# Optimization experiments

Measured on AMD Instinct MI355X. Metric: run time of the kernel, lower is better.

## Reference

```python
import jax, jax.numpy as jnp
import numpy as np

B = 32
H = W = 64
C = 128
HEADS = 4
HEAD_DIM = C // HEADS
WS = 8            # window_size
SS = 4            # shift_size
N = WS * WS       # tokens per window
MLP_HID = 4 * C
SCALE = HEAD_DIM ** -0.5
EPS = 1e-5


def _rel_pos_index():
    coords = np.stack(np.meshgrid(np.arange(WS), np.arange(WS), indexing='ij'))
    cf = coords.reshape(2, -1)
    rel = (cf[:, :, None] - cf[:, None, :]).transpose(1, 2, 0)
    rel[:, :, 0] += WS - 1
    rel[:, :, 1] += WS - 1
    rel[:, :, 0] *= 2 * WS - 1
    return rel.sum(-1)  # (N, N) int


def _attn_mask():
    img_mask = np.zeros((1, H, W, 1), np.float32)
    slices = (slice(0, -WS), slice(-WS, -SS), slice(-SS, None))
    cnt = 0
    for hs in slices:
        for ws in slices:
            img_mask[:, hs, ws, :] = cnt
            cnt += 1
    mw = img_mask.reshape(1, H // WS, WS, W // WS, WS, 1)
    mw = mw.transpose(0, 1, 3, 2, 4, 5).reshape(-1, N)  # (nW, N)
    am = mw[:, None, :] - mw[:, :, None]
    return np.where(am != 0, np.float32(-100.0), np.float32(0.0))  # (nW, N, N)


REL_POS_IDX = jnp.asarray(_rel_pos_index().reshape(-1))  # (N*N,)
ATTN_MASK = jnp.asarray(_attn_mask())                    # (nW, N, N)


def setup_inputs() -> dict:
    key = jax.random.key(0)
    ks = jax.random.split(key, 12)
    s = 0.02
    return {
        'x': jax.random.normal(ks[0], (B, H * W, C), jnp.float32),
        'norm1_g': jnp.ones((C,), jnp.float32),
        'norm1_b': jnp.zeros((C,), jnp.float32),
        'qkv_w': jax.random.normal(ks[1], (C, 3 * C), jnp.float32) * s,
        'qkv_b': jnp.zeros((3 * C,), jnp.float32),
        'proj_w': jax.random.normal(ks[2], (C, C), jnp.float32) * s,
        'proj_b': jnp.zeros((C,), jnp.float32),
        'rpb_table': jax.random.normal(ks[3], ((2 * WS - 1) * (2 * WS - 1), HEADS), jnp.float32) * s,
        'norm2_g': jnp.ones((C,), jnp.float32),
        'norm2_b': jnp.zeros((C,), jnp.float32),
        'mlp_w1': jax.random.normal(ks[4], (C, MLP_HID), jnp.float32) * s,
        'mlp_b1': jnp.zeros((MLP_HID,), jnp.float32),
        'mlp_w2': jax.random.normal(ks[5], (MLP_HID, C), jnp.float32) * s,
        'mlp_b2': jnp.zeros((C,), jnp.float32),
    }


def _layernorm(x, g, b):
    m = x.mean(-1, keepdims=True)
    v = jnp.mean((x - m) ** 2, -1, keepdims=True)
    return (x - m) * jax.lax.rsqrt(v + EPS) * g + b


def reference(x, norm1_g, norm1_b, qkv_w, qkv_b, proj_w, proj_b, rpb_table,
              norm2_g, norm2_b, mlp_w1, mlp_b1, mlp_w2, mlp_b2):
    shortcut = x
    h = _layernorm(x, norm1_g, norm1_b).reshape(-1, H, W, C)
    # cyclic shift
    h = jnp.roll(h, (-SS, -SS), axis=(1, 2))
    # window partition -> (B*nW, N, C)
    hw = h.reshape(-1, H // WS, WS, W // WS, WS, C)
    hw = hw.transpose(0, 1, 3, 2, 4, 5).reshape(-1, N, C)
    # window attention
    qkv = (hw @ qkv_w + qkv_b).reshape(-1, N, 3, HEADS, HEAD_DIM)
    qkv = qkv.transpose(2, 0, 3, 1, 4)  # (3, B*nW, heads, N, hd)
    q, k, v = qkv[0] * SCALE, qkv[1], qkv[2]
    attn = jnp.einsum('bhnd,bhmd->bhnm', q, k)  # (B*nW, heads, N, N)
    rpb = rpb_table[REL_POS_IDX].reshape(N, N, HEADS).transpose(2, 0, 1)
    attn = attn + rpb[None]
    nW = ATTN_MASK.shape[0]
    attn = attn.reshape(-1, nW, HEADS, N, N) + ATTN_MASK[None, :, None]
    attn = jax.nn.softmax(attn.reshape(-1, HEADS, N, N), axis=-1)
    out = jnp.einsum('bhnm,bhmd->bhnd', attn, v)
    out = out.transpose(0, 2, 1, 3).reshape(-1, N, C)
    out = out @ proj_w + proj_b
    # window reverse
    out = out.reshape(-1, H // WS, W // WS, WS, WS, C)
    out = out.transpose(0, 1, 3, 2, 4, 5).reshape(-1, H, W, C)
    # reverse cyclic shift
    out = jnp.roll(out, (SS, SS), axis=(1, 2)).reshape(-1, H * W, C)
    x = shortcut + out
    # MLP branch
    h2 = _layernorm(x, norm2_g, norm2_b)
    h2 = jax.nn.gelu(h2 @ mlp_w1 + mlp_b1, approximate=False)
    h2 = h2 @ mlp_w2 + mlp_b2
    return x + h2
```

## Files before the change

kernel.cpp:

```cpp
#include <hip/hip_runtime.h>
#include <math.h>

typedef __attribute__((ext_vector_type(8))) short bf16x8;
typedef __attribute__((ext_vector_type(4))) short bf16x4;
typedef __attribute__((ext_vector_type(4))) float f32x4;
typedef __attribute__((ext_vector_type(4))) unsigned short u16x4;

#define DEVI __device__ __forceinline__

DEVI float b2f(unsigned int u){ union{unsigned int i; float f;} c; c.i = u<<16; return c.f; }
DEVI unsigned short f2b(float f){
  union{float f; unsigned int i;} c; c.f = f;
  unsigned int r = c.i + 0x7fffu + ((c.i>>16)&1u);
  return (unsigned short)(r>>16);
}
DEVI unsigned int pack2(float a, float b){
  return (unsigned int)f2b(a) | ((unsigned int)f2b(b)<<16);
}
DEVI void unpack8(uint4 u, float* f){
  f[0]=b2f(u.x&0xffffu); f[1]=b2f(u.x>>16);
  f[2]=b2f(u.y&0xffffu); f[3]=b2f(u.y>>16);
  f[4]=b2f(u.z&0xffffu); f[5]=b2f(u.z>>16);
  f[6]=b2f(u.w&0xffffu); f[7]=b2f(u.w>>16);
}
DEVI f32x4 mfma16(bf16x8 a, bf16x8 b, f32x4 c){
  return __builtin_amdgcn_mfma_f32_16x16x32_bf16(a, b, c, 0, 0, 0);
}
DEVI f32x4 mfma16x16(bf16x4 a, bf16x4 b, f32x4 c){
#if __has_builtin(__builtin_amdgcn_mfma_f32_16x16x16bf16_1k)
  return __builtin_amdgcn_mfma_f32_16x16x16bf16_1k(a, b, c, 0, 0, 0);
#else
  f32x4 d = c;
  asm volatile("v_mfma_f32_16x16x16_bf16 %0, %1, %2, %0" : "+v"(d) : "v"(a), "v"(b));
  return d;
#endif
}
DEVI float gelu_fast(float u){
  const float y = 0.7978845608028654f*(u + 0.044715f*u*u*u);
  const float t = __expf(2.f*y);
  const float th = 1.f - 2.f/(t + 1.f);
  return 0.5f*u*(1.f + th);
}
DEVI int swzA(int row, int byi){ return row*256 + (byi ^ ((row&7)<<4)); }
DEVI int swzQ(int row, int byi){ return row*64  + (byi ^ (((row>>1)&3)<<4)); }
DEVI int swzO(int row, int byc){ return row*512 + (byc ^ ((row&7)<<4) ^ (((byc>>7)&3)<<5)); }

__global__ void k_prep(const float* __restrict__ qkvw, const float* __restrict__ projw,
                       const float* __restrict__ w1,   const float* __restrict__ w2,
                       const float* __restrict__ rpbt,
                       ushort* __restrict__ qkvF, ushort* __restrict__ projF,
                       ushort* __restrict__ w1F,  ushort* __restrict__ w2F,
                       ushort* __restrict__ rpbE)
{
  const int t = blockIdx.x*256 + threadIdx.x;
  const int l = t&63, fr = t>>6;
  const int l15 = l&15, l4 = l>>4;
  {
    const int head = t>>12, q = (t>>6)&63, k = t&63;
    const int di = (q>>3)-(k>>3)+7, dj = (q&7)-(k&7)+7;
    rpbE[t] = f2b(rpbt[(di*15+dj)*4 + head]);
  }
  {
    const int c = fr>>5, og = (fr>>2)&7, h = fr&3;
    const int oc = og*16 + l15, hid0 = c*64 + h*16 + l4*4;
    ushort* d = w2F + (size_t)fr*256 + l*4;
    #pragma unroll
    for(int e=0;e<4;e++) d[e] = f2b(w2[(size_t)(hid0+e)*128 + oc]);
  }
  if (fr < 128){
    const int c = fr>>4, hg = (fr>>2)&3, kk = fr&3;
    const int hid = c*64 + hg*16 + l15, k0 = kk*32 + l4*8;
    ushort* d = w1F + (size_t)fr*512 + l*8;
    #pragma unroll
    for(int e=0;e<8;e++) d[e] = f2b(w1[(size_t)(k0+e)*512 + hid]);
  }
  if (fr < 96){
    const int s3 = fr>>5, g = (fr>>2)&7, kk = fr&3;
    const int col = s3*128 + g*16 + l15, k0 = kk*32 + l4*8;
    ushort* d = qkvF + (size_t)fr*512 + l*8;
    #pragma unroll
    for(int e=0;e<8;e++) d[e] = f2b(qkvw[(size_t)(k0+e)*384 + col]);
  }
  if (fr < 32){
    const int g = fr>>2, kk = fr&3;
    const int col = g*16 + l15, k0 = kk*32 + l4*8;
    ushort* d = projF + (size_t)fr*512 + l*8;
    #pragma unroll
    for(int e=0;e<8;e++) d[e] = f2b(projw[(size_t)(k0+e)*128 + col]);
  }
}

__global__ __launch_bounds__(256,3) void k_attn(
    const float*  __restrict__ x,
    const float*  __restrict__ g1, const float* __restrict__ be1,
    const ushort* __restrict__ qkvF, const float* __restrict__ qkvb,
    const ushort* __restrict__ projF, const float* __restrict__ projb,
    const ushort* __restrict__ rpbE,
    ushort* __restrict__ x2w)
{
  __shared__ __align__(16) char smem[49152];
  const int tid  = threadIdx.x;
  const int wave = tid>>6, lane = tid&63;
  const int l15 = lane&15, l4 = lane>>4;
  const int wid = blockIdx.x;
  const int b   = wid>>6, wim = wid&63;
  const int wh  = wim>>3, wv = wim&7;

  char* const smA  = smem;
  char* const smQ  = smem + 16384 + wave*8192;
  char* const smK  = smQ + 4096;
  char* const smR  = smem + 16384;

  const f32x4 Z = {0.f,0.f,0.f,0.f};
  const int t_row = tid>>2;
  const int cg    = (tid&3)*32;
  const int ti_r = t_row>>3, tj_r = t_row&7;
  const int ho_r = (wh*8+ti_r+4)&63, wo_r = (wv*8+tj_r+4)&63;
  const size_t growbase = ((size_t)(b*4096 + ho_r*64 + wo_r))*128;

  {
    const float* src = x + growbase + cg;
    float v[32];
    #pragma unroll
    for(int q=0;q<8;q++){
      const float4 f4 = *(const float4*)(src + q*4);
      v[q*4+0]=f4.x; v[q*4+1]=f4.y; v[q*4+2]=f4.z; v[q*4+3]=f4.w;
    }
    float s=0.f, ss=0.f;
    #pragma unroll
    for(int e=0;e<32;e++){ s+=v[e]; ss+=v[e]*v[e]; }
    s += __shfl_xor(s,1); ss += __shfl_xor(ss,1);
    s += __shfl_xor(s,2); ss += __shfl_xor(ss,2);
    const float mean = s*(1.f/128.f);
    const float varv = fmaxf(ss*(1.f/128.f) - mean*mean, 0.f);
    const float rstd = rsqrtf(varv + 1e-5f);
    #pragma unroll
    for(int q=0;q<4;q++){
      const float4 ga = *(const float4*)(g1 +cg+q*8);
      const float4 gb = *(const float4*)(g1 +cg+q*8+4);
      const float4 ba = *(const float4*)(be1+cg+q*8);
      const float4 bb = *(const float4*)(be1+cg+q*8+4);
      const float* vp = v + q*8;
      uint4 pk;
      pk.x = pack2((vp[0]-mean)*rstd*ga.x+ba.x, (vp[1]-mean)*rstd*ga.y+ba.y);
      pk.y = pack2((vp[2]-mean)*rstd*ga.z+ba.z, (vp[3]-mean)*rstd*ga.w+ba.w);
      pk.z = pack2((vp[4]-mean)*rstd*gb.x+bb.x, (vp[5]-mean)*rstd*gb.y+bb.y);
      pk.w = pack2((vp[6]-mean)*rstd*gb.z+bb.z, (vp[7]-mean)*rstd*gb.w+bb.w);
      *(uint4*)(smA + swzA(t_row, cg*2 + q*16)) = pk;
    }
  }
  __syncthreads();

  const int headc = wave*32;
  bf16x4 Vf[4][2];

  {
    #pragma unroll
    for(int s3=0;s3<3;s3++){
      f32x4 acc[4][2];
      #pragma unroll
      for(int rt=0;rt<4;rt++){ acc[rt][0]=Z; acc[rt][1]=Z; }
      bf16x8 bfr[2][4];
      #pragma unroll
      for(int ct=0;ct<2;ct++)
        #pragma unroll
        for(int kk=0;kk<4;kk++)
          bfr[ct][kk] = *(const bf16x8*)(qkvF + (size_t)((s3*8 + wave*2 + ct)*4 + kk)*512 + lane*8);
      #pragma unroll
      for(int kk=0;kk<4;kk++){
        bf16x8 afr[4];
        #pragma unroll
        for(int rt=0;rt<4;rt++)
          afr[rt] = *(const bf16x8*)(smA + swzA(rt*16+l15, kk*64 + l4*16));
        #pragma unroll
        for(int rt=0;rt<4;rt++)
          #pragma unroll
          for(int ct=0;ct<2;ct++)
            acc[rt][ct] = mfma16(afr[rt], bfr[ct][kk], acc[rt][ct]);
      }
      #pragma unroll
      for(int ct=0;ct<2;ct++){
        const int hd = ct*16 + l15;
        const float bias = qkvb[s3*128 + headc + hd];
        if (s3==2){
          #pragma unroll
          for(int rt=0;rt<4;rt++){
            union { uint2 u; bf16x4 v; } cv;
            cv.u.x = pack2(acc[rt][ct][0]+bias, acc[rt][ct][1]+bias);
            cv.u.y = pack2(acc[rt][ct][2]+bias, acc[rt][ct][3]+bias);
            Vf[rt][ct] = cv.v;
          }
        } else {
          char* const dst = (s3==0) ? smQ : smK;
          const float sc = (s3==0) ? 0.17677669529663687f : 1.f;
          #pragma unroll
          for(int rt=0;rt<4;rt++){
            const int t0 = rt*16 + l4*4;
            #pragma unroll
            for(int j=0;j<4;j++)
              *(ushort*)(dst + swzQ(t0+j, hd*2)) = f2b((acc[rt][ct][j]+bias)*sc);
          }
        }
      }
    }
  }
  __syncthreads();

  f32x4 O[4][2];
  #pragma unroll
  for(int rt=0;rt<4;rt++){ O[rt][0]=Z; O[rt][1]=Z; }
  {
    bf16x8 kfr[4];
    #pragma unroll
    for(int g=0; g<4; ++g)
      kfr[g] = *(const bf16x8*)(smK + swzQ(g*16+l15, l4*16));
    const bool edge = (wh==7) || (wv==7);
    #pragma unroll
    for(int rt=0; rt<4; ++rt){
      const bf16x8 qf = *(const bf16x8*)(smQ + swzQ(rt*16+l15, l4*16));
      f32x4 S[4];
      #pragma unroll
      for(int g=0; g<4; ++g)
        S[g] = mfma16(kfr[g], qf, Z);
      const int q = rt*16 + l15;
      int regq = 0;
      if (edge){
        const int qi=q>>3, qj=q&7;
        regq = ((wh<7)?0:((qi<4)?1:2))*3 + ((wv<7)?0:((qj<4)?1:2));
      }
      const ushort* rbase = rpbE + wave*4096 + q*64 + l4*4;
      #pragma unroll
      for(int g=0; g<4; ++g){
        const u16x4 rb = *(const u16x4*)(rbase + g*16);
        #pragma unroll
        for(int j=0;j<4;j++){
          float add = b2f(rb[j]);
          if (edge){
            const int k = g*16 + l4*4 + j;
            const int ki=k>>3, kj=k&7;
            const int regk = ((wh<7)?0:((ki<4)?1:2))*3 + ((wv<7)?0:((kj<4)?1:2));
            if (regk != regq) add -= 100.f;
          }
          S[g][j] += add;
        }
      }
      float mx = -1e30f;
      #pragma unroll
      for(int g=0;g<4;g++)
        #pragma unroll
        for(int j=0;j<4;j++) mx = fmaxf(mx, S[g][j]);
      mx = fmaxf(mx, __shfl_xor(mx,16));
      mx = fmaxf(mx, __shfl_xor(mx,32));
      float sm = 0.f;
      #pragma unroll
      for(int g=0;g<4;g++)
        #pragma unroll
        for(int j=0;j<4;j++){ const float e = __expf(S[g][j]-mx); S[g][j]=e; sm+=e; }
      sm += __shfl_xor(sm,16);
      sm += __shfl_xor(sm,32);
      const float inv = 1.f/sm;
      #pragma unroll
      for(int g=0;g<4;g++){
        union { uint2 u; bf16x4 v; } cv;
        cv.u.x = pack2(S[g][0]*inv, S[g][1]*inv);
        cv.u.y = pack2(S[g][2]*inv, S[g][3]*inv);
        #pragma unroll
        for(int cvi=0;cvi<2;cvi++)
          O[rt][cvi] = mfma16x16(cv.v, Vf[g][cvi], O[rt][cvi]);
      }
    }
    #pragma unroll
    for(int rt=0;rt<4;rt++)
      #pragma unroll
      for(int cvi=0;cvi<2;cvi++)
        #pragma unroll
        for(int j=0;j<4;j++)
          *(ushort*)(smA + swzA(rt*16+l4*4+j, (headc + cvi*16 + l15)*2)) = f2b(O[rt][cvi][j]);
  }
  __syncthreads();

  {
    f32x4 PR[4][2];
    #pragma unroll
    for(int rt=0;rt<4;rt++){ PR[rt][0]=Z; PR[rt][1]=Z; }
    bf16x8 pb[2][4];
    #pragma unroll
    for(int ct=0;ct<2;ct++)
      #pragma unroll
      for(int kk=0;kk<4;kk++)
        pb[ct][kk] = *(const bf16x8*)(projF + (size_t)((wave*2+ct)*4 + kk)*512 + lane*8);
    #pragma unroll
    for(int kk=0;kk<4;kk++){
      bf16x8 afr[4];
      #pragma unroll
      for(int rt=0;rt<4;rt++)
        afr[rt] = *(const bf16x8*)(smA + swzA(rt*16+l15, kk*64 + l4*16));
      #pragma unroll
      for(int rt=0;rt<4;rt++)
        #pragma unroll
        for(int ct=0;ct<2;ct++)
          PR[rt][ct] = mfma16(afr[rt], pb[ct][kk], PR[rt][ct]);
    }
    #pragma unroll
    for(int ct=0;ct<2;ct++){
      const int col = headc + ct*16 + l15;
      const float bias = projb[col];
      #pragma unroll
      for(int rt=0;rt<4;rt++)
        #pragma unroll
        for(int j=0;j<4;j++)
          *(float*)(smR + swzO(rt*16+l4*4+j, col*4)) = PR[rt][ct][j] + bias;
    }
  }
  __syncthreads();

  {
    const float* xsrc = x + growbase + cg;
    ushort* drow = x2w + ((size_t)(wid*64 + t_row))*128 + cg;
    #pragma unroll
    for(int q=0;q<4;q++){
      const f32x4 oa = *(const f32x4*)(smR + swzO(t_row, (cg+q*8  )*4));
      const f32x4 ob = *(const f32x4*)(smR + swzO(t_row, (cg+q*8+4)*4));
      const float4 xa = *(const float4*)(xsrc + q*8);
      const float4 xb = *(const float4*)(xsrc + q*8+4);
      uint4 pk;
      pk.x = pack2(oa[0]+xa.x, oa[1]+xa.y);
      pk.y = pack2(oa[2]+xa.z, oa[3]+xa.w);
      pk.z = pack2(ob[0]+xb.x, ob[1]+xb.y);
      pk.w = pack2(ob[2]+xb.z, ob[3]+xb.w);
      *(uint4*)(drow + q*8) = pk;
    }
  }
}

__global__ __launch_bounds__(512,1) void k_mlp2(
    const ushort* __restrict__ x2w,
    const float* __restrict__ g2, const float* __restrict__ be2,
    const ushort* __restrict__ w1F, const float* __restrict__ bb1,
    const ushort* __restrict__ w2F, const float* __restrict__ bb2,
    float* __restrict__ outp)
{
  extern __shared__ __align__(16) char smem[];
  char* const smX  = smem;
  char* const smW0 = smem + 65536;
  char* const smW1 = smem + 98304;
  const int tid  = threadIdx.x;
  const int wave = tid>>6, lane = tid&63;
  const int l15 = lane&15, l4 = lane>>4;
  const int gblk = blockIdx.x;
  const f32x4 Z = {0.f,0.f,0.f,0.f};

  const ushort* const wsrc = (tid & 256) ? w2F : w1F;
  const int soff = (tid & 255) * 32;
  const int loff = ((tid & 256) ? 16384 : 0) + (tid & 255)*64;
  uint4 stg0, stg1, stg2, stg3;
  {
    const uint4* p = (const uint4*)(wsrc + soff);
    stg0 = p[0]; stg1 = p[1]; stg2 = p[2]; stg3 = p[3];
  }

  {
    const int sub = tid>>2;
    const int cg  = (tid&3)*32;
    #pragma unroll
    for(int p=0;p<2;++p){
      const int tk = p*128 + sub;
      const ushort* src = x2w + ((size_t)(gblk*256 + tk))*128 + cg;
      float v[32];
      unpack8(*(const uint4*)(src   ), v   );
      unpack8(*(const uint4*)(src+ 8), v+ 8);
      unpack8(*(const uint4*)(src+16), v+16);
      unpack8(*(const uint4*)(src+24), v+24);
      float s=0.f, ss=0.f;
      #pragma unroll
      for(int e=0;e<32;e++){ s+=v[e]; ss+=v[e]*v[e]; }
      s += __shfl_xor(s,1); ss += __shfl_xor(ss,1);
      s += __shfl_xor(s,2); ss += __shfl_xor(ss,2);
      const float mean = s*(1.f/128.f);
      const float varv = fmaxf(ss*(1.f/128.f) - mean*mean, 0.f);
      const float rstd = rsqrtf(varv + 1e-5f);
      #pragma unroll
      for(int q=0;q<4;q++){
        const float4 ga = *(const float4*)(g2 +cg+q*8);
        const float4 gb = *(const float4*)(g2 +cg+q*8+4);
        const float4 ba = *(const float4*)(be2+cg+q*8);
        const float4 bb = *(const float4*)(be2+cg+q*8+4);
        const float* vp = v + q*8;
        uint4 pk;
        pk.x = pack2((vp[0]-mean)*rstd*ga.x+ba.x, (vp[1]-mean)*rstd*ga.y+ba.y);
        pk.y = pack2((vp[2]-mean)*rstd*ga.z+ba.z, (vp[3]-mean)*rstd*ga.w+ba.w);
        pk.z = pack2((vp[4]-mean)*rstd*gb.x+bb.x, (vp[5]-mean)*rstd*gb.y+bb.y);
        pk.w = pack2((vp[6]-mean)*rstd*gb.z+bb.z, (vp[7]-mean)*rstd*gb.w+bb.w);
        *(uint4*)(smX + swzA(tk, cg*2 + q*16)) = pk;
      }
    }
  }
  {
    uint4* d = (uint4*)(smW0 + loff);
    d[0]=stg0; d[1]=stg1; d[2]=stg2; d[3]=stg3;
  }
  __syncthreads();

  f32x4 OA[8][2];
  #pragma unroll
  for(int ocg=0;ocg<8;++ocg){ OA[ocg][0]=Z; OA[ocg][1]=Z; }

  for (int c=0; c<8; ++c){
    char* const buf = (c&1) ? smW1 : smW0;
    if (c<7){
      const uint4* p = (const uint4*)(wsrc + (size_t)(c+1)*8192 + soff);
      stg0 = p[0]; stg1 = p[1]; stg2 = p[2]; stg3 = p[3];
    }
    const int hidb = c*64;
    #pragma unroll
    for (int tokg=0; tokg<2; ++tokg){
      const int trow = wave*32 + tokg*16 + l15;
      bf16x8 xf[4];
      #pragma unroll
      for(int kk=0;kk<4;++kk)
        xf[kk] = *(const bf16x8*)(smX + swzA(trow, kk*64 + l4*16));
      f32x4 acc1[4] = {Z,Z,Z,Z};
      #pragma unroll
      for(int hg=0; hg<4; ++hg)
        #pragma unroll
        for(int kk=0; kk<4; ++kk){
          const bf16x8 wf = *(const bf16x8*)(buf + (hg*4+kk)*1024 + lane*16);
          acc1[hg] = mfma16(wf, xf[kk], acc1[hg]);
        }
      bf16x4 Hf[4];
      #pragma unroll
      for(int hg=0; hg<4; ++hg){
        const float4 b4 = *(const float4*)(bb1 + hidb + hg*16 + l4*4);
        bf16x4 hv;
        hv[0] = (short)f2b(gelu_fast(acc1[hg][0]+b4.x));
        hv[1] = (short)f2b(gelu_fast(acc1[hg][1]+b4.y));
        hv[2] = (short)f2b(gelu_fast(acc1[hg][2]+b4.z));
        hv[3] = (short)f2b(gelu_fast(acc1[hg][3]+b4.w));
        Hf[hg] = hv;
      }
      #pragma unroll
      for(int ocg=0; ocg<8; ++ocg)
        #pragma unroll
        for(int hg=0; hg<4; ++hg){
          const bf16x4 w2f = *(const bf16x4*)(buf + 16384 + (ocg*4+hg)*512 + lane*8);
          OA[ocg][tokg] = mfma16x16(w2f, Hf[hg], OA[ocg][tokg]);
        }
    }
    if (c<7){
      char* const nbuf = (c&1) ? smW0 : smW1;
      uint4* d = (uint4*)(nbuf + loff);
      d[0]=stg0; d[1]=stg1; d[2]=stg2; d[3]=stg3;
    }
    __syncthreads();
  }

  {
    const int sub = tid>>2;
    const int cg  = (tid&3)*32;
    #pragma unroll
    for(int p=0;p<2;++p){
      const int tk = p*128 + sub;
      const uint4* src = (const uint4*)(x2w + ((size_t)(gblk*256 + tk))*128 + cg);
      #pragma unroll
      for(int q=0;q<4;q++) *(uint4*)(smX + swzA(tk, cg*2 + q*16)) = src[q];
    }
  }
  __syncthreads();
  #pragma unroll
  for(int tokg=0; tokg<2; ++tokg){
    const int tk  = wave*32 + tokg*16 + l15;
    const int wid = gblk*4 + (tk>>6);
    const int n   = tk & 63;
    const int bb  = wid>>6, wim = wid&63;
    const int wh  = wim>>3, wv = wim&7;
    const int ti  = n>>3,  tj = n&7;
    const int ho  = (wh*8+ti+4)&63, wo = (wv*8+tj+4)&63;
    float* const drow = outp + ((size_t)(bb*4096 + ho*64 + wo))*128;
    #pragma unroll
    for(int ocg=0; ocg<8; ++ocg){
      const int oc = ocg*16 + l4*4;
      const float4 b4 = *(const float4*)(bb2 + oc);
      const u16x4 xr = *(const u16x4*)(smX + swzA(tk, oc*2));
      f32x4 r = OA[ocg][tokg];
      r[0] += b4.x + b2f(xr[0]);
      r[1] += b4.y + b2f(xr[1]);
      r[2] += b4.z + b2f(xr[2]);
      r[3] += b4.w + b2f(xr[3]);
      __builtin_nontemporal_store(r, (f32x4*)(drow + oc));
    }
  }
}

extern "C" void kernel_launch(void* const* d_in, const int* in_sizes, int n_in,
                              void* d_out, int out_size, void* d_ws, size_t ws_size,
                              hipStream_t stream) {
  (void)in_sizes; (void)n_in; (void)out_size; (void)ws_size;
  const float* x     = (const float*)d_in[0];
  const float* n1g   = (const float*)d_in[1];
  const float* n1b   = (const float*)d_in[2];
  const float* qkvw  = (const float*)d_in[3];
  const float* qkvb  = (const float*)d_in[4];
  const float* projw = (const float*)d_in[5];
  const float* projb = (const float*)d_in[6];
  const float* rpbt  = (const float*)d_in[7];
  const float* n2g   = (const float*)d_in[8];
  const float* n2b   = (const float*)d_in[9];
  const float* w1    = (const float*)d_in[10];
  const float* b1    = (const float*)d_in[11];
  const float* w2    = (const float*)d_in[12];
  const float* b2    = (const float*)d_in[13];
  float* outp = (float*)d_out;

  ushort* ws    = (ushort*)d_ws;
  ushort* x2w   = ws;
  ushort* qkvF  = ws + 16777216;
  ushort* projF = qkvF + 49152;
  ushort* w1F   = projF + 16384;
  ushort* w2F   = w1F + 65536;
  ushort* rpbE  = w2F + 65536;

  k_prep<<<64, 256, 0, stream>>>(qkvw, projw, w1, w2, rpbt, qkvF, projF, w1F, w2F, rpbE);
  k_attn<<<2048, 256, 0, stream>>>(x, n1g, n1b, qkvF, qkvb, projF, projb, rpbE, x2w);
  k_mlp2<<<512, 512, 131072, stream>>>(x2w, n2g, n2b, w1F, b1, w2F, b2, outp);
}
```

Before: 188.1 us.

## Cut MLP kernel LDS to 64KB using direct global-to-LDS weight staging

The MLP kernel now holds its normalized activation fragments in registers instead of re-reading them from shared memory. That frees the activation region so the weight double-buffers can reuse it, and shared memory drops from 128KB to 64KB per block. Weight chunks are streamed with global_load_lds straight into LDS, with a prefetch distance of two chunks, instead of staging through registers. This aims to allow more blocks per CU and to drop the register staging, at the cost of extra register pressure and an added barrier per chunk.

Result: slower. 237.3 us (+26.2%).

```diff
diff --git a/kernel.cpp b/kernel.cpp
--- a/kernel.cpp
+++ b/kernel.cpp
@@ -333,31 +333,19 @@
   }
 }
 
-__global__ __launch_bounds__(512,1) void k_mlp2(
+__global__ __launch_bounds__(512,4) void k_mlp2(
     const ushort* __restrict__ x2w,
     const float* __restrict__ g2, const float* __restrict__ be2,
     const ushort* __restrict__ w1F, const float* __restrict__ bb1,
     const ushort* __restrict__ w2F, const float* __restrict__ bb2,
     float* __restrict__ outp)
 {
-  extern __shared__ __align__(16) char smem[];
-  char* const smX  = smem;
-  char* const smW0 = smem + 65536;
-  char* const smW1 = smem + 98304;
+  __shared__ __align__(16) char smem[65536];
   const int tid  = threadIdx.x;
   const int wave = tid>>6, lane = tid&63;
   const int l15 = lane&15, l4 = lane>>4;
   const int gblk = blockIdx.x;
   const f32x4 Z = {0.f,0.f,0.f,0.f};
-
-  const ushort* const wsrc = (tid & 256) ? w2F : w1F;
-  const int soff = (tid & 255) * 32;
-  const int loff = ((tid & 256) ? 16384 : 0) + (tid & 255)*64;
-  uint4 stg0, stg1, stg2, stg3;
-  {
-    const uint4* p = (const uint4*)(wsrc + soff);
-    stg0 = p[0]; stg1 = p[1]; stg2 = p[2]; stg3 = p[3];
-  }
 
   {
     const int sub = tid>>2;
@@ -391,41 +379,54 @@
         pk.y = pack2((vp[2]-mean)*rstd*ga.z+ba.z, (vp[3]-mean)*rstd*ga.w+ba.w);
         pk.z = pack2((vp[4]-mean)*rstd*gb.x+bb.x, (vp[5]-mean)*rstd*gb.y+bb.y);
         pk.w = pack2((vp[6]-mean)*rstd*gb.z+bb.z, (vp[7]-mean)*rstd*gb.w+bb.w);
-        *(uint4*)(smX + swzA(tk, cg*2 + q*16)) = pk;
-      }
-    }
-  }
-  {
-    uint4* d = (uint4*)(smW0 + loff);
-    d[0]=stg0; d[1]=stg1; d[2]=stg2; d[3]=stg3;
-  }
-  __syncthreads();
+        *(uint4*)(smem + swzA(tk, cg*2 + q*16)) = pk;
+      }
+    }
+  }
+  __syncthreads();
+
+  bf16x8 xf[2][4];
+  #pragma unroll
+  for(int tokg=0;tokg<2;++tokg){
+    const int trow = wave*32 + tokg*16 + l15;
+    #pragma unroll
+    for(int kk=0;kk<4;++kk)
+      xf[tokg][kk] = *(const bf16x8*)(smem + swzA(trow, kk*64 + l4*16));
+  }
+  __syncthreads();
+
+  const ushort* const wsrc = (wave<4) ? w1F : w2F;
+  const int ldsoff = ((wave<4)?0:16384) + (wave&3)*4096;
+  const int subsh  = (wave&3)*2048;
+  #define STAGE_CHUNK(cc, bufbase) do{ \
+    const ushort* gsrc = wsrc + (size_t)(cc)*8192 + subsh + lane*8; \
+    char* lb = (bufbase) + ldsoff; \
+    __builtin_amdgcn_global_load_lds((const unsigned int*)(gsrc      ), (unsigned int*)(lb       ), 16, 0, 0); \
+    __builtin_amdgcn_global_load_lds((const unsigned int*)(gsrc+ 512 ), (unsigned int*)(lb+1024  ), 16, 0, 0); \
+    __builtin_amdgcn_global_load_lds((const unsigned int*)(gsrc+1024 ), (unsigned int*)(lb+2048  ), 16, 0, 0); \
+    __builtin_amdgcn_global_load_lds((const unsigned int*)(gsrc+1536 ), (unsigned int*)(lb+3072  ), 16, 0, 0); \
+  }while(0)
+
+  STAGE_CHUNK(0, smem);
+  STAGE_CHUNK(1, smem + 32768);
 
   f32x4 OA[8][2];
   #pragma unroll
   for(int ocg=0;ocg<8;++ocg){ OA[ocg][0]=Z; OA[ocg][1]=Z; }
 
   for (int c=0; c<8; ++c){
-    char* const buf = (c&1) ? smW1 : smW0;
-    if (c<7){
-      const uint4* p = (const uint4*)(wsrc + (size_t)(c+1)*8192 + soff);
-      stg0 = p[0]; stg1 = p[1]; stg2 = p[2]; stg3 = p[3];
-    }
+    __syncthreads();
+    char* const buf = (c&1) ? (smem + 32768) : smem;
     const int hidb = c*64;
     #pragma unroll
     for (int tokg=0; tokg<2; ++tokg){
-      const int trow = wave*32 + tokg*16 + l15;
-      bf16x8 xf[4];
-      #pragma unroll
-      for(int kk=0;kk<4;++kk)
-        xf[kk] = *(const bf16x8*)(smX + swzA(trow, kk*64 + l4*16));
       f32x4 acc1[4] = {Z,Z,Z,Z};
       #pragma unroll
       for(int hg=0; hg<4; ++hg)
         #pragma unroll
         for(int kk=0; kk<4; ++kk){
           const bf16x8 wf = *(const bf16x8*)(buf + (hg*4+kk)*1024 + lane*16);
-          acc1[hg] = mfma16(wf, xf[kk], acc1[hg]);
+          acc1[hg] = mfma16(wf, xf[tokg][kk], acc1[hg]);
         }
       bf16x4 Hf[4];
       #pragma unroll
@@ -446,13 +447,10 @@
           OA[ocg][tokg] = mfma16x16(w2f, Hf[hg], OA[ocg][tokg]);
         }
     }
-    if (c<7){
-      char* const nbuf = (c&1) ? smW0 : smW1;
-      uint4* d = (uint4*)(nbuf + loff);
-      d[0]=stg0; d[1]=stg1; d[2]=stg2; d[3]=stg3;
-    }
     __syncthreads();
-  }
+    if (c < 6) STAGE_CHUNK(c+2, (c&1) ? (smem + 32768) : smem);
+  }
+  #undef STAGE_CHUNK
 
   {
     const int sub = tid>>2;
@@ -462,7 +460,7 @@
       const int tk = p*128 + sub;
       const uint4* src = (const uint4*)(x2w + ((size_t)(gblk*256 + tk))*128 + cg);
       #pragma unroll
-      for(int q=0;q<4;q++) *(uint4*)(smX + swzA(tk, cg*2 + q*16)) = src[q];
+      for(int q=0;q<4;q++) *(uint4*)(smem + swzA(tk, cg*2 + q*16)) = src[q];
     }
   }
   __syncthreads();
@@ -480,7 +478,7 @@
     for(int ocg=0; ocg<8; ++ocg){
       const int oc = ocg*16 + l4*4;
       const float4 b4 = *(const float4*)(bb2 + oc);
-      const u16x4 xr = *(const u16x4*)(smX + swzA(tk, oc*2));
+      const u16x4 xr = *(const u16x4*)(smem + swzA(tk, oc*2));
       f32x4 r = OA[ocg][tokg];
       r[0] += b4.x + b2f(xr[0]);
       r[1] += b4.y + b2f(xr[1]);
@@ -521,5 +519,5 @@
 
   k_prep<<<64, 256, 0, stream>>>(qkvw, projw, w1, w2, rpbt, qkvF, projF, w1F, w2F, rpbE);
   k_attn<<<2048, 256, 0, stream>>>(x, n1g, n1b, qkvF, qkvb, projF, projb, rpbE, x2w);
-  k_mlp2<<<512, 512, 131072, stream>>>(x2w, n2g, n2b, w1F, b1, w2F, b2, outp);
-}
+  k_mlp2<<<512, 512, 0, stream>>>(x2w, n2g, n2b, w1F, b1, w2F, b2, outp);
+}
```
